# Optimization experiments

Measured on AMD Instinct MI355X. Metric: run time of the kernel, lower is better.

Reference implementation:

```python
import jax, jax.numpy as jnp
import numpy as np

NUM_HEADS = 16
HEAD_DIM = 128
EMBED = NUM_HEADS * HEAD_DIM  # 2048
BATCH, SEQ = 2, 2048


def setup_inputs() -> dict:
    key = jax.random.key(0)
    k1, k2 = jax.random.split(key)
    x = jax.random.normal(k1, (BATCH, SEQ, EMBED), dtype=jnp.float32)
    W = jax.random.normal(k2, (EMBED, 3 * EMBED), dtype=jnp.float32) * 0.02
    b = jnp.zeros((3 * EMBED,), dtype=jnp.float32)
    return {"x": x, "W": W, "b": b}


def _rotate_half(u):
    u1, u2 = jnp.split(u, 2, axis=-1)
    return jnp.concatenate([-u2, u1], axis=-1)


def reference(x, W, b):
    B, S, E = x.shape
    H, D = NUM_HEADS, HEAD_DIM
    # Fused QKV projection: [B,S,E] @ [E,3E] -> [B,S,3E]
    qkv = jnp.einsum('bse,ef->bsf', x, W) + b
    qkv = qkv.reshape(B, S, 3, H, D)
    q, k, v = qkv[:, :, 0], qkv[:, :, 1], qkv[:, :, 2]  # each [B,S,H,D]
    # Module's rotary embedding: sin/cos over arange(S*D), shared across heads
    t = jnp.arange(S * D, dtype=jnp.float32).reshape(1, S, 1, D)
    sin, cos = jnp.sin(t), jnp.cos(t)
    q = q * cos + _rotate_half(q) * sin
    k = k * cos + _rotate_half(k) * sin
    # Scaled dot-product attention over sequence, per head
    scale = 1.0 / jnp.sqrt(jnp.float32(D))
    attn = jnp.einsum('bqhd,bkhd->bhqk', q, k) * scale  # [B,H,S,S]
    w = jax.nn.softmax(attn, axis=-1)
    out = jnp.einsum('bhqk,bkhd->bqhd', w, v)  # [B,S,H,D]
    return out
```

## Files before the change

kernel.cpp:

```cpp
#include <hip/hip_runtime.h>
#include <stdint.h>

typedef unsigned short u16;
typedef __attribute__((ext_vector_type(8))) short bf16x8;
typedef __attribute__((ext_vector_type(4))) float f32x4;

#define NUM_B 2
#define SEQ   2048
#define SEQP  2080
#define NH    16
#define HD    128
#define EMB   2048
#define N3    6144
#define MM    4096
#define QT    64
#define WQ    32
#define KT    32
#define NTILE (SEQ / KT)

#define BM 256
#define BN 256
#define BK 64
#define NT_K (EMB / BK)

__device__ __forceinline__ u16 f2bf(float f) {
  union { float f; unsigned u; } c; c.f = f;
  return (u16)((c.u + 0x7FFFu + ((c.u >> 16) & 1u)) >> 16);
}
__device__ __forceinline__ void async16(const void* g, void* l) {
  __builtin_amdgcn_global_load_lds(
      (const __attribute__((address_space(1))) void*)g,
      (__attribute__((address_space(3))) void*)l, 16, 0, 0);
}

#define GBAR()   asm volatile("s_barrier" ::: "memory")
#define WLGKM0() asm volatile("s_waitcnt lgkmcnt(0)" ::: "memory")


__global__ void k_cvt_bf16(const float* __restrict__ in, u16* __restrict__ out, int n4) {
  int i = blockIdx.x * blockDim.x + threadIdx.x;
  if (i >= n4) return;
  const float4 v = ((const float4*)in)[i];
  ushort4 o;
  o.x = f2bf(v.x); o.y = f2bf(v.y); o.z = f2bf(v.z); o.w = f2bf(v.w);
  ((ushort4*)out)[i] = o;
}

__global__ void k_transpose_w(const float* __restrict__ W, u16* __restrict__ Wt) {
  __shared__ float t[32][33];
  int n0 = blockIdx.x * 32, k0 = blockIdx.y * 32;
  int tx = threadIdx.x, ty = threadIdx.y;
  #pragma unroll
  for (int i = ty; i < 32; i += 8)
    t[i][tx] = W[(size_t)(k0 + i) * N3 + n0 + tx];
  __syncthreads();
  #pragma unroll
  for (int i = ty; i < 32; i += 8)
    Wt[(size_t)(n0 + i) * EMB + k0 + tx] = f2bf(t[tx][i]);
}

__global__ void k_sincos(float2* __restrict__ tab) {
  int i = blockIdx.x * blockDim.x + threadIdx.x;
  double t = (double)i;
  tab[i] = make_float2((float)cos(t), (float)sin(t));
}

__global__ __launch_bounds__(512, 2) void k_gemm_qkv(
    const u16* __restrict__ xb, const u16* __restrict__ wt,
    const float* __restrict__ bias, const float2* __restrict__ tab,
    u16* __restrict__ qb, u16* __restrict__ kb, u16* __restrict__ vbt)
{
  __shared__ __align__(16) u16 lsA[2][BM * BK];
  __shared__ __align__(16) u16 lsB[2][BN * BK];
  const int tid = threadIdx.x;
  const int wave = tid >> 6, lane = tid & 63;
  const int lq = lane & 15, lr = lane >> 4;
  const int wr = wave >> 2, wc = wave & 3;
  const int m0 = blockIdx.y * BM, n0 = blockIdx.x * BN;

  auto stA = [&](int t, int half) {
    const int kt = t * BK;
    #pragma unroll
    for (int ii = 0; ii < 2; ++ii) {
      int s = ii * 512 + tid;
      int row = s >> 3, gq = (s & 7) ^ (row & 7);
      async16(xb + (size_t)(m0 + half * 128 + row) * EMB + kt + gq * 8,
              &lsA[t & 1][half * 8192 + s * 8]);
    }
  };
  auto stB = [&](int t, int half) {
    const int kt = t * BK;
    #pragma unroll
    for (int ii = 0; ii < 2; ++ii) {
      int s = ii * 512 + tid;
      int row = s >> 3, gq = (s & 7) ^ (row & 7);
      async16(wt + (size_t)(n0 + half * 128 + row) * EMB + kt + gq * 8,
              &lsB[t & 1][half * 8192 + s * 8]);
    }
  };

  f32x4 acc[8][4];
  #pragma unroll
  for (int i = 0; i < 8; ++i)
    #pragma unroll
    for (int j = 0; j < 4; ++j)
      acc[i][j] = f32x4{0.f, 0.f, 0.f, 0.f};

  int rbase[4];
  #pragma unroll
  for (int nf = 0; nf < 4; ++nf)
    rbase[nf] = ((wc >> 1) * 128 + (2 * (wc & 1) + (nf >> 1)) * 16 + (nf & 1) * 64 + lq) * BK;
  const int aRow0 = (wr * 128 + lq) * BK;
  int qsw[2];
  qsw[0] = ((0 + lr) ^ (lq & 7)) * 8;
  qsw[1] = ((4 + lr) ^ (lq & 7)) * 8;

  stA(0, 0); stA(0, 1); stB(0, 0); stB(0, 1); stB(1, 0); stB(1, 1);
  asm volatile("s_waitcnt vmcnt(4)" ::: "memory");
  GBAR();

  for (int ti = 0; ti < NT_K / 2; ++ti) {
    const int t0 = 2 * ti, t1 = t0 + 1;
    const bool notlast = (ti < NT_K / 2 - 1);

    #pragma unroll
    for (int hp = 0; hp < 2; ++hp) {
      const u16* Ap = lsA[hp];
      const u16* Bp = lsB[hp];
      bf16x8 bfr[4][2];

      #pragma unroll
      for (int q = 0; q < 4; ++q) {
        if (q == 0) {
          #pragma unroll
          for (int nf = 0; nf < 4; ++nf)
            #pragma unroll
            for (int kk = 0; kk < 2; ++kk)
              bfr[nf][kk] = *(const bf16x8*)(Bp + rbase[nf] + qsw[kk]);
        }
        bf16x8 af[2][2];
        #pragma unroll
        for (int mfl = 0; mfl < 2; ++mfl)
          #pragma unroll
          for (int kk = 0; kk < 2; ++kk)
            af[mfl][kk] = *(const bf16x8*)(Ap + aRow0 + (q * 32 + mfl * 16) * BK + qsw[kk]);

        if (hp == 0) {
          if      (q == 0) stA(t1, 0);
          else if (q == 1) stA(t1, 1);
          else if (q == 2) { if (notlast) stB(t0 + 2, 0); }
          else {
            if (notlast) {
              stB(t0 + 2, 1);
              asm volatile("s_waitcnt vmcnt(4)" ::: "memory");
            } else {
              asm volatile("s_waitcnt vmcnt(0)" ::: "memory");
            }
          }
        } else {
          if      (q == 0) { if (notlast) stA(t0 + 2, 0); }
          else if (q == 1) { if (notlast) stA(t0 + 2, 1); }
          else if (q == 2) { if (notlast) stB(t1 + 2, 0); }
          else {
            if (notlast) {
              stB(t1 + 2, 1);
              asm volatile("s_waitcnt vmcnt(4)" ::: "memory");
            }
          }
        }
        if (q == 0) asm volatile("s_waitcnt lgkmcnt(8)" ::: "memory");

        GBAR();
        WLGKM0();
        __builtin_amdgcn_s_setprio(1);
        #pragma unroll
        for (int kk = 0; kk < 2; ++kk)
          #pragma unroll
          for (int mfl = 0; mfl < 2; ++mfl)
            #pragma unroll
            for (int nf = 0; nf < 4; ++nf)
              acc[q * 2 + mfl][nf] = __builtin_amdgcn_mfma_f32_16x16x32_bf16(
                  af[mfl][kk], bfr[nf][kk], acc[q * 2 + mfl][nf], 0, 0, 0);
        __builtin_amdgcn_s_setprio(0);
        GBAR();
      }
    }
  }

  const int w = n0 >> 11;
  const int h = ((n0 & 2047) >> 7) + (wc >> 1);
  float bb[4];
  int dloc[4];
  #pragma unroll
  for (int nf = 0; nf < 4; ++nf) {
    dloc[nf] = (2 * (wc & 1) + (nf >> 1)) * 16 + (nf & 1) * 64 + lq;
    bb[nf] = bias[n0 + (wc >> 1) * 128 + dloc[nf]];
  }

  if (w == 2) {
    #pragma unroll
    for (int mf = 0; mf < 8; ++mf) {
      int mg0 = m0 + wr * 128 + mf * 16 + lr * 4;
      int b = mg0 >> 11, s0 = mg0 & 2047;
      #pragma unroll
      for (int nf = 0; nf < 4; ++nf) {
        int d = dloc[nf];
        ushort4 pk;
        pk.x = f2bf(acc[mf][nf][0] + bb[nf]);
        pk.y = f2bf(acc[mf][nf][1] + bb[nf]);
        pk.z = f2bf(acc[mf][nf][2] + bb[nf]);
        pk.w = f2bf(acc[mf][nf][3] + bb[nf]);
        *(ushort4*)(vbt + ((size_t)(b * NH + h) * HD + d) * SEQP + s0) = pk;
      }
    }
  } else {
    u16* basep = (w == 0) ? qb : kb;
    const float qs = (w == 0) ? 0.12751569843736827f : 1.0f;
    #pragma unroll
    for (int mf = 0; mf < 8; ++mf)
      #pragma unroll
      for (int r = 0; r < 4; ++r) {
        int mg = m0 + wr * 128 + mf * 16 + lr * 4 + r;
        int b = mg >> 11, s = mg & 2047;
        u16* dst = basep + ((size_t)(b * NH + h) * SEQ + s) * HD;
        #pragma unroll
        for (int pl = 0; pl < 2; ++pl) {
          int d1 = (2 * (wc & 1) + pl) * 16 + lq;
          float c1 = acc[mf][2 * pl][r]     + bb[2 * pl];
          float c2 = acc[mf][2 * pl + 1][r] + bb[2 * pl + 1];
          float2 s1 = tab[s * HD + d1];
          float2 s2 = tab[s * HD + d1 + 64];
          dst[d1]      = f2bf((c1 * s1.x - c2 * s1.y) * qs);
          dst[d1 + 64] = f2bf((c2 * s2.x + c1 * s2.y) * qs);
        }
      }
  }
}

__global__ __launch_bounds__(128, 2) void k_flash(
    const u16* __restrict__ qb, const u16* __restrict__ kb,
    const u16* __restrict__ vbt, float* __restrict__ out)
{
  __shared__ __align__(16) u16 lsK[2][KT * HD];
  __shared__ __align__(16) u16 lsV[2][HD * KT];
  __shared__ __align__(16) u16 lsP[2][WQ * KT];

  const int tid = threadIdx.x;
  const int wave = tid >> 6, lane = tid & 63;
  const int lq = lane & 15, lr = lane >> 4;
  const int i = blockIdx.x;
  const int xcd = i & 7, j = i >> 3;
  const int bh = xcd * 4 + (j >> 5);
  const int q0 = (j & 31) * QT;
  const u16* Qg = qb + ((size_t)bh * SEQ + q0 + wave * WQ) * HD;
  const u16* Kg = kb + (size_t)bh * SEQ * HD;
  const u16* Vg = vbt + (size_t)bh * HD * SEQP;

  auto stage = [&](int tile, int buf) {
    const int k0 = tile * KT;
    #pragma unroll
    for (int ii = 0; ii < 4; ++ii) {
      int c = tid + ii * 128;
      int key = c >> 4, grp = c & 15;
      async16(Kg + (size_t)(k0 + key) * HD + ((grp ^ (key & 7)) * 8), lsK[buf] + c * 8);
    }
    #pragma unroll
    for (int ii = 0; ii < 4; ++ii) {
      int c = tid + ii * 128;
      int d = c >> 2, g2 = c & 3;
      async16(Vg + (size_t)d * SEQP + k0 + ((g2 ^ ((d >> 1) & 3)) * 8), lsV[buf] + c * 8);
    }
  };

  stage(0, 0);

  bf16x8 qf[2][4];
  #pragma unroll
  for (int qq = 0; qq < 2; ++qq)
    #pragma unroll
    for (int ks = 0; ks < 4; ++ks)
      qf[qq][ks] = *(const bf16x8*)(Qg + (size_t)(qq * 16 + lq) * HD + ks * 32 + lr * 8);

  f32x4 acc_o[2][8];
  float lsum[2] = {0.f, 0.f};
  #pragma unroll
  for (int mb = 0; mb < 2; ++mb)
    #pragma unroll
    for (int nb = 0; nb < 8; ++nb) acc_o[mb][nb] = f32x4{0.f, 0.f, 0.f, 0.f};

  for (int t = 0; t < NTILE; ++t) {
    const int p = t & 1;
    __syncthreads();
    if (t + 1 < NTILE) stage(t + 1, 1 - p);

    f32x4 sacc[2][2];
    #pragma unroll
    for (int kbi = 0; kbi < 2; ++kbi)
      #pragma unroll
      for (int qq = 0; qq < 2; ++qq) sacc[kbi][qq] = f32x4{0.f, 0.f, 0.f, 0.f};
    #pragma unroll
    for (int ks = 0; ks < 4; ++ks) {
      bf16x8 kf[2];
      #pragma unroll
      for (int kbi = 0; kbi < 2; ++kbi) {
        int key = kbi * 16 + lq;
        int g = (ks * 4 + lr) ^ (key & 7);
        kf[kbi] = *(const bf16x8*)(lsK[p] + key * HD + g * 8);
      }
      #pragma unroll
      for (int kbi = 0; kbi < 2; ++kbi)
        #pragma unroll
        for (int qq = 0; qq < 2; ++qq)
          sacc[kbi][qq] = __builtin_amdgcn_mfma_f32_16x16x32_bf16(kf[kbi], qf[qq][ks], sacc[kbi][qq], 0, 0, 0);
    }

    #pragma unroll
    for (int kbi = 0; kbi < 2; ++kbi)
      #pragma unroll
      for (int qq = 0; qq < 2; ++qq) {
        float p0 = __builtin_amdgcn_exp2f(sacc[kbi][qq][0]);
        float p1 = __builtin_amdgcn_exp2f(sacc[kbi][qq][1]);
        float p2 = __builtin_amdgcn_exp2f(sacc[kbi][qq][2]);
        float p3 = __builtin_amdgcn_exp2f(sacc[kbi][qq][3]);
        lsum[qq] += (p0 + p1) + (p2 + p3);
        int row = qq * 16 + lq;
        int g = kbi * 4 + lr;
        int gp = g ^ (row & 6);
        uint2 pk;
        pk.x = (uint32_t)f2bf(p0) | ((uint32_t)f2bf(p1) << 16);
        pk.y = (uint32_t)f2bf(p2) | ((uint32_t)f2bf(p3) << 16);
        *(uint2*)(lsP[wave] + row * KT + gp * 4) = pk;
      }

    bf16x8 ap[2];
    #pragma unroll
    for (int mb = 0; mb < 2; ++mb) {
      int row = mb * 16 + lq;
      int gp = (2 * lr) ^ (row & 6);
      ap[mb] = *(const bf16x8*)(lsP[wave] + row * KT + gp * 4);
    }
    #pragma unroll
    for (int nb = 0; nb < 8; ++nb) {
      int d = nb * 16 + lq;
      int g2 = lr ^ ((d >> 1) & 3);
      bf16x8 bv = *(const bf16x8*)(lsV[p] + d * KT + g2 * 8);
      #pragma unroll
      for (int mb = 0; mb < 2; ++mb)
        acc_o[mb][nb] = __builtin_amdgcn_mfma_f32_16x16x32_bf16(ap[mb], bv[0] == bv[0] ? bv : bv, acc_o[mb][nb], 0, 0, 0);
    }
  }

  float inv[2];
  #pragma unroll
  for (int qq = 0; qq < 2; ++qq) {
    float s = lsum[qq];
    s += __shfl_xor(s, 16);
    s += __shfl_xor(s, 32);
    inv[qq] = 1.0f / s;
  }
  const int b = bh >> 4, h = bh & 15;
  #pragma unroll
  for (int mb = 0; mb < 2; ++mb)
    #pragma unroll
    for (int r = 0; r < 4; ++r) {
      float iv = __shfl(inv[mb], lr * 4 + r);
      int row = wave * WQ + mb * 16 + lr * 4 + r;
      int sq = q0 + row;
      float* op = out + (((size_t)b * SEQ + sq) * NH + h) * HD;
      #pragma unroll
      for (int nb = 0; nb < 8; ++nb)
        op[nb * 16 + lq] = acc_o[mb][nb][r] * iv;
    }
}


extern "C" void kernel_launch(void* const* d_in, const int* in_sizes, int n_in,
                              void* d_out, int out_size, void* d_ws, size_t ws_size,
                              hipStream_t stream) {
  (void)in_sizes; (void)n_in; (void)out_size; (void)ws_size;
  const float* x    = (const float*)d_in[0];
  const float* W    = (const float*)d_in[1];
  const float* bias = (const float*)d_in[2];
  float* out = (float*)d_out;

  char* p = (char*)d_ws;
  u16* xb  = (u16*)p;  p += (size_t)MM * EMB * 2;
  u16* wt  = (u16*)p;  p += (size_t)N3 * EMB * 2;
  u16* qb  = (u16*)p;  p += (size_t)NUM_B * NH * SEQ * HD * 2;
  u16* kb  = (u16*)p;  p += (size_t)NUM_B * NH * SEQ * HD * 2;
  u16* vbt = (u16*)p;  p += (size_t)NUM_B * NH * HD * SEQP * 2;
  float2* tab = (float2*)p;

  k_cvt_bf16<<<(MM * EMB / 4 + 255) / 256, 256, 0, stream>>>(x, xb, MM * EMB / 4);
  k_transpose_w<<<dim3(N3 / 32, EMB / 32), dim3(32, 8), 0, stream>>>(W, wt);
  k_sincos<<<(SEQ * HD) / 256, 256, 0, stream>>>(tab);
  k_gemm_qkv<<<dim3(N3 / BN, MM / BM), 512, 0, stream>>>(xb, wt, bias, tab, qb, kb, vbt);
  k_flash<<<SEQ / QT * NUM_B * NH, 128, 0, stream>>>(qb, kb, vbt, out);
}
```

Baseline: 245.8 us.

## Widen QKV GEMM tile to 256x384 for a single full wave of blocks

Raises the QKV GEMM N-tile from 256 to 384, so each block covers three heads. This gives 16x16 = 256 blocks instead of 384, removing the partial second wave on a 256-CU part. The inner loop is rebuilt around six B fragments per wave with a new per-phase prefetch and waitcnt schedule. The epilogue now iterates over three head slices per wave to apply bias, RoPE and scale. Shared memory use grows to about 160KB and launch bounds drop to one block per CU, which raises register pressure from the larger accumulator array.

Measured after the change: 384.5 us. 56.5% more time.

```diff
diff --git a/kernel.cpp b/kernel.cpp
--- a/kernel.cpp
+++ b/kernel.cpp
@@ -19,7 +19,7 @@
 #define NTILE (SEQ / KT)
 
 #define BM 256
-#define BN 256
+#define BN 384
 #define BK 64
 #define NT_K (EMB / BK)
 
@@ -65,7 +65,7 @@
   tab[i] = make_float2((float)cos(t), (float)sin(t));
 }
 
-__global__ __launch_bounds__(512, 2) void k_gemm_qkv(
+__global__ __launch_bounds__(512, 1) void k_gemm_qkv(
     const u16* __restrict__ xb, const u16* __restrict__ wt,
     const float* __restrict__ bias, const float2* __restrict__ tab,
     u16* __restrict__ qb, u16* __restrict__ kb, u16* __restrict__ vbt)
@@ -88,152 +88,149 @@
               &lsA[t & 1][half * 8192 + s * 8]);
     }
   };
-  auto stB = [&](int t, int half) {
+  auto stB = [&](int t, int third) {
     const int kt = t * BK;
     #pragma unroll
     for (int ii = 0; ii < 2; ++ii) {
       int s = ii * 512 + tid;
       int row = s >> 3, gq = (s & 7) ^ (row & 7);
-      async16(wt + (size_t)(n0 + half * 128 + row) * EMB + kt + gq * 8,
-              &lsB[t & 1][half * 8192 + s * 8]);
+      async16(wt + (size_t)(n0 + third * 128 + row) * EMB + kt + gq * 8,
+              &lsB[t & 1][third * 8192 + s * 8]);
     }
   };
 
-  f32x4 acc[8][4];
+  f32x4 acc[8][6];
   #pragma unroll
   for (int i = 0; i < 8; ++i)
     #pragma unroll
-    for (int j = 0; j < 4; ++j)
+    for (int j = 0; j < 6; ++j)
       acc[i][j] = f32x4{0.f, 0.f, 0.f, 0.f};
 
-  int rbase[4];
-  #pragma unroll
-  for (int nf = 0; nf < 4; ++nf)
-    rbase[nf] = ((wc >> 1) * 128 + (2 * (wc & 1) + (nf >> 1)) * 16 + (nf & 1) * 64 + lq) * BK;
+  int rbase[6];
+  #pragma unroll
+  for (int nf = 0; nf < 6; ++nf) {
+    int pi = 3 * wc + (nf >> 1);
+    int o = (pi >> 2) * 128 + (pi & 3) * 16 + (nf & 1) * 64;
+    rbase[nf] = (o + lq) * BK;
+  }
   const int aRow0 = (wr * 128 + lq) * BK;
   int qsw[2];
   qsw[0] = ((0 + lr) ^ (lq & 7)) * 8;
   qsw[1] = ((4 + lr) ^ (lq & 7)) * 8;
 
-  stA(0, 0); stA(0, 1); stB(0, 0); stB(0, 1); stB(1, 0); stB(1, 1);
-  asm volatile("s_waitcnt vmcnt(4)" ::: "memory");
+  stA(0, 0); stA(0, 1); stB(0, 0); stB(0, 1); stB(0, 2); stB(1, 0);
+  asm volatile("s_waitcnt vmcnt(2)" ::: "memory");
   GBAR();
 
   for (int ti = 0; ti < NT_K / 2; ++ti) {
     const int t0 = 2 * ti, t1 = t0 + 1;
-    const bool notlast = (ti < NT_K / 2 - 1);
+    const bool nl = (ti < NT_K / 2 - 1);
 
     #pragma unroll
     for (int hp = 0; hp < 2; ++hp) {
       const u16* Ap = lsA[hp];
       const u16* Bp = lsB[hp];
-      bf16x8 bfr[4][2];
-
-      #pragma unroll
-      for (int q = 0; q < 4; ++q) {
-        if (q == 0) {
+      bf16x8 bfr[6];
+
+      #pragma unroll
+      for (int p = 0; p < 4; ++p) {
+        const int kk = p >> 1, mh = p & 1;
+        if (mh == 0) {
           #pragma unroll
-          for (int nf = 0; nf < 4; ++nf)
-            #pragma unroll
-            for (int kk = 0; kk < 2; ++kk)
-              bfr[nf][kk] = *(const bf16x8*)(Bp + rbase[nf] + qsw[kk]);
+          for (int nf = 0; nf < 6; ++nf)
+            bfr[nf] = *(const bf16x8*)(Bp + rbase[nf] + qsw[kk]);
         }
-        bf16x8 af[2][2];
+        bf16x8 af[4];
         #pragma unroll
-        for (int mfl = 0; mfl < 2; ++mfl)
-          #pragma unroll
-          for (int kk = 0; kk < 2; ++kk)
-            af[mfl][kk] = *(const bf16x8*)(Ap + aRow0 + (q * 32 + mfl * 16) * BK + qsw[kk]);
+        for (int m4 = 0; m4 < 4; ++m4)
+          af[m4] = *(const bf16x8*)(Ap + aRow0 + ((mh * 4 + m4) * 16) * BK + qsw[kk]);
 
         if (hp == 0) {
-          if      (q == 0) stA(t1, 0);
-          else if (q == 1) stA(t1, 1);
-          else if (q == 2) { if (notlast) stB(t0 + 2, 0); }
-          else {
-            if (notlast) {
-              stB(t0 + 2, 1);
-              asm volatile("s_waitcnt vmcnt(4)" ::: "memory");
+          if      (p == 0) { stA(t1, 0); stB(t1, 1); }
+          else if (p == 1) { stA(t1, 1); stB(t1, 2); }
+          else if (p == 3) {
+            if (nl) {
+              stB(t0 + 2, 0);
+              asm volatile("s_waitcnt vmcnt(2)" ::: "memory");
             } else {
               asm volatile("s_waitcnt vmcnt(0)" ::: "memory");
             }
           }
         } else {
-          if      (q == 0) { if (notlast) stA(t0 + 2, 0); }
-          else if (q == 1) { if (notlast) stA(t0 + 2, 1); }
-          else if (q == 2) { if (notlast) stB(t1 + 2, 0); }
-          else {
-            if (notlast) {
-              stB(t1 + 2, 1);
-              asm volatile("s_waitcnt vmcnt(4)" ::: "memory");
+          if (nl) {
+            if      (p == 0) { stA(t0 + 2, 0); stB(t0 + 2, 1); }
+            else if (p == 1) { stA(t0 + 2, 1); stB(t0 + 2, 2); }
+            else if (p == 3) {
+              stB(t1 + 2, 0);
+              asm volatile("s_waitcnt vmcnt(2)" ::: "memory");
             }
           }
         }
-        if (q == 0) asm volatile("s_waitcnt lgkmcnt(8)" ::: "memory");
+        if (mh == 0) asm volatile("s_waitcnt lgkmcnt(4)" ::: "memory");
 
         GBAR();
         WLGKM0();
         __builtin_amdgcn_s_setprio(1);
         #pragma unroll
-        for (int kk = 0; kk < 2; ++kk)
+        for (int m4 = 0; m4 < 4; ++m4)
           #pragma unroll
-          for (int mfl = 0; mfl < 2; ++mfl)
-            #pragma unroll
-            for (int nf = 0; nf < 4; ++nf)
-              acc[q * 2 + mfl][nf] = __builtin_amdgcn_mfma_f32_16x16x32_bf16(
-                  af[mfl][kk], bfr[nf][kk], acc[q * 2 + mfl][nf], 0, 0, 0);
+          for (int nf = 0; nf < 6; ++nf)
+            acc[mh * 4 + m4][nf] = __builtin_amdgcn_mfma_f32_16x16x32_bf16(
+                af[m4], bfr[nf], acc[mh * 4 + m4][nf], 0, 0, 0);
         __builtin_amdgcn_s_setprio(0);
         GBAR();
       }
     }
   }
 
-  const int w = n0 >> 11;
-  const int h = ((n0 & 2047) >> 7) + (wc >> 1);
-  float bb[4];
-  int dloc[4];
-  #pragma unroll
-  for (int nf = 0; nf < 4; ++nf) {
-    dloc[nf] = (2 * (wc & 1) + (nf >> 1)) * 16 + (nf & 1) * 64 + lq;
-    bb[nf] = bias[n0 + (wc >> 1) * 128 + dloc[nf]];
-  }
-
-  if (w == 2) {
-    #pragma unroll
-    for (int mf = 0; mf < 8; ++mf) {
-      int mg0 = m0 + wr * 128 + mf * 16 + lr * 4;
-      int b = mg0 >> 11, s0 = mg0 & 2047;
-      #pragma unroll
-      for (int nf = 0; nf < 4; ++nf) {
-        int d = dloc[nf];
+  const int m0w = m0 + wr * 128;
+  #pragma unroll
+  for (int pl = 0; pl < 3; ++pl) {
+    const int pi = 3 * wc + pl;
+    const int j = pi >> 2;
+    const int H = (n0 >> 7) + j;
+    const int w = H >> 4;
+    const int h = H & 15;
+    const int poff = (pi & 3) * 16;
+    const float b1 = bias[n0 + j * 128 + poff + lq];
+    const float b2 = bias[n0 + j * 128 + poff + 64 + lq];
+
+    if (w == 2) {
+      #pragma unroll
+      for (int mf = 0; mf < 8; ++mf) {
+        int mg0 = m0w + mf * 16 + lr * 4;
+        int b = mg0 >> 11, s0 = mg0 & 2047;
         ushort4 pk;
-        pk.x = f2bf(acc[mf][nf][0] + bb[nf]);
-        pk.y = f2bf(acc[mf][nf][1] + bb[nf]);
-        pk.z = f2bf(acc[mf][nf][2] + bb[nf]);
-        pk.w = f2bf(acc[mf][nf][3] + bb[nf]);
-        *(ushort4*)(vbt + ((size_t)(b * NH + h) * HD + d) * SEQP + s0) = pk;
+        pk.x = f2bf(acc[mf][2 * pl][0] + b1);
+        pk.y = f2bf(acc[mf][2 * pl][1] + b1);
+        pk.z = f2bf(acc[mf][2 * pl][2] + b1);
+        pk.w = f2bf(acc[mf][2 * pl][3] + b1);
+        *(ushort4*)(vbt + ((size_t)(b * NH + h) * HD + poff + lq) * SEQP + s0) = pk;
+        pk.x = f2bf(acc[mf][2 * pl + 1][0] + b2);
+        pk.y = f2bf(acc[mf][2 * pl + 1][1] + b2);
+        pk.z = f2bf(acc[mf][2 * pl + 1][2] + b2);
+        pk.w = f2bf(acc[mf][2 * pl + 1][3] + b2);
+        *(ushort4*)(vbt + ((size_t)(b * NH + h) * HD + poff + 64 + lq) * SEQP + s0) = pk;
       }
-    }
-  } else {
-    u16* basep = (w == 0) ? qb : kb;
-    const float qs = (w == 0) ? 0.12751569843736827f : 1.0f;
-    #pragma unroll
-    for (int mf = 0; mf < 8; ++mf)
-      #pragma unroll
-      for (int r = 0; r < 4; ++r) {
-        int mg = m0 + wr * 128 + mf * 16 + lr * 4 + r;
-        int b = mg >> 11, s = mg & 2047;
-        u16* dst = basep + ((size_t)(b * NH + h) * SEQ + s) * HD;
+    } else {
+      u16* basep = (w == 0) ? qb : kb;
+      const float qs = (w == 0) ? 0.12751569843736827f : 1.0f;
+      #pragma unroll
+      for (int mf = 0; mf < 8; ++mf)
         #pragma unroll
-        for (int pl = 0; pl < 2; ++pl) {
-          int d1 = (2 * (wc & 1) + pl) * 16 + lq;
-          float c1 = acc[mf][2 * pl][r]     + bb[2 * pl];
-          float c2 = acc[mf][2 * pl + 1][r] + bb[2 * pl + 1];
+        for (int r = 0; r < 4; ++r) {
+          int mg = m0w + mf * 16 + lr * 4 + r;
+          int b = mg >> 11, s = mg & 2047;
+          u16* dst = basep + ((size_t)(b * NH + h) * SEQ + s) * HD;
+          int d1 = poff + lq;
+          float c1 = acc[mf][2 * pl][r]     + b1;
+          float c2 = acc[mf][2 * pl + 1][r] + b2;
           float2 s1 = tab[s * HD + d1];
           float2 s2 = tab[s * HD + d1 + 64];
           dst[d1]      = f2bf((c1 * s1.x - c2 * s1.y) * qs);
           dst[d1 + 64] = f2bf((c2 * s2.x + c1 * s2.y) * qs);
         }
-      }
+    }
   }
 }
 
```
